# Kernel optimization log

Measured on AMD Instinct MI355X. Metric: run time of the kernel, lower is better.

The kernel has to match this reference:

```python
import jax, jax.numpy as jnp
import numpy as np

B, N, K = 4, 4096, 16
C_IN = 128
EPS = 1e-5


def setup_inputs() -> dict:
    key = jax.random.key(0)
    ks = jax.random.split(key, 8)
    c0 = 2 * C_IN + 3  # concat channels: pos_diff(3) + feat2(128) + feat1(128)
    return {
        "pos1": jax.random.normal(ks[0], (B, 3, N), jnp.float32),
        "pos2": jax.random.normal(ks[1], (B, 3, N), jnp.float32),
        "feature1": jax.random.normal(ks[2], (B, C_IN, N), jnp.float32),
        "feature2": jax.random.normal(ks[3], (B, C_IN, N), jnp.float32),
        "W0": jax.random.normal(ks[4], (128, c0), jnp.float32) * 0.05,
        "W1": jax.random.normal(ks[5], (128, 128), jnp.float32) * 0.05,
        "W2": jax.random.normal(ks[6], (128, 128), jnp.float32) * 0.05,
        "g0": jnp.ones((128,), jnp.float32),
        "g1": jnp.ones((128,), jnp.float32),
        "g2": jnp.ones((128,), jnp.float32),
        "b0": jnp.zeros((128,), jnp.float32),
        "b1": jnp.zeros((128,), jnp.float32),
        "b2": jnp.zeros((128,), jnp.float32),
    }


def _knn_idx(pos1, pos2, k):
    # pos1, pos2: (B, 3, N).  For each point in pos1, k nearest points in pos2.
    p1 = pos1.transpose(0, 2, 1)  # (B, N, 3)
    p2 = pos2.transpose(0, 2, 1)  # (B, M, 3)
    d = (jnp.sum(p1 * p1, -1, keepdims=True)
         + jnp.sum(p2 * p2, -1)[:, None, :]
         - 2.0 * jnp.einsum("bnc,bmc->bnm", p1, p2))  # (B, N, M) squared dists
    _, idx = jax.lax.top_k(-d, k)  # (B, N, K)
    return idx


def _group(x, idx):
    # x: (B, C, M), idx: (B, N, K) -> (B, C, N, K)
    xt = x.transpose(0, 2, 1)  # (B, M, C)
    g = jax.vmap(lambda a, i: a[i])(xt, idx)  # (B, N, K, C)
    return g.transpose(0, 3, 1, 2)


def _conv_bn_relu(x, W, g, b):
    # 1x1 conv (no bias) + BatchNorm2d (training: batch stats, biased var) + ReLU
    y = jnp.einsum("oc,bcnk->bonk", W, x)
    mu = jnp.mean(y, axis=(0, 2, 3), keepdims=True)
    var = jnp.var(y, axis=(0, 2, 3), keepdims=True)
    yn = (y - mu) * jax.lax.rsqrt(var + EPS)
    return jax.nn.relu(yn * g[None, :, None, None] + b[None, :, None, None])


def reference(pos1, pos2, feature1, feature2, W0, W1, W2, g0, g1, g2, b0, b1, b2):
    idx = _knn_idx(pos1, pos2, K)                      # (B, N, K)
    pos2_g = _group(pos2, idx)                         # (B, 3, N, K)
    pos_diff = pos2_g - pos1[:, :, :, None]
    feat2_g = _group(feature2, idx)                    # (B, C, N, K)
    feat1_rep = jnp.broadcast_to(feature1[:, :, :, None], (B, C_IN, N, K))
    x = jnp.concatenate([pos_diff, feat2_g, feat1_rep], axis=1)  # (B, 2C+3, N, K)
    x = _conv_bn_relu(x, W0, g0, b0)
    x = _conv_bn_relu(x, W1, g1, b1)
    x = _conv_bn_relu(x, W2, g2, b2)
    feat1_new = jnp.max(x, axis=-1)                    # (B, mlp[-1], N)
    return (pos1, feat1_new)
```

## Files before the change

### kernel.cpp

```cpp
#include <hip/hip_runtime.h>

#define B_ 4
#define N_ 4096
#define K_ 16
#define C_ 128
#define NQ (B_*N_)
#define COLS_TOT (NQ*K_)
#define CNT_F 262144.0f
#define EPS_ 1e-5f

typedef __attribute__((ext_vector_type(8))) short short8;
typedef __attribute__((ext_vector_type(4))) float f4;
typedef __attribute__((ext_vector_type(4))) int i4;

__device__ __forceinline__ unsigned short f2bf(float f){
  unsigned u = __builtin_bit_cast(unsigned, f);
  u = u + 0x7fffu + ((u >> 16) & 1u);
  return (unsigned short)(u >> 16);
}
__device__ __forceinline__ float bf2f(unsigned short h){
  return __builtin_bit_cast(float, ((unsigned)h) << 16);
}
__device__ __forceinline__ int swzc(int c){ return c ^ ((c >> 3) & 7); }

__global__ __launch_bounds__(256) void wconv(
    const float* __restrict__ W0, const float* __restrict__ W1, const float* __restrict__ W2,
    unsigned short* __restrict__ W0b, unsigned short* __restrict__ W0c,
    unsigned short* __restrict__ W1b, unsigned short* __restrict__ W2b)
{
  int i = blockIdx.x * 256 + threadIdx.x;
  int sel = i >> 14, r = i & 16383;
  int o = r >> 7, c = r & 127;
  float v; unsigned short* dst;
  if (sel == 0)      { v = W0[o*259 + 3   + c]; dst = W0b; }
  else if (sel == 1) { v = W0[o*259 + 131 + c]; dst = W0c; }
  else if (sel == 2) { v = W1[o*128 + c];       dst = W1b; }
  else               { v = W2[o*128 + c];       dst = W2b; }
  dst[r] = f2bf(v);
}

__global__ __launch_bounds__(256) void knn_chunk(
    const float* __restrict__ pos1, const float* __restrict__ pos2,
    float* __restrict__ kdout, int* __restrict__ kiout)
{
  __shared__ __align__(16) float pts[256*4];
  int bx = blockIdx.x;
  int b = bx >> 8, rest = bx & 255, ngrp = rest >> 4, chunk = rest & 15;
  int t = threadIdx.x;
  int m0 = chunk * 256;
  const float* p2 = pos2 + (size_t)b*3*N_;
  {
    int m = m0 + t;
    float x = p2[m], y = p2[N_ + m], z = p2[2*N_ + m];
    float sq = __fadd_rn(__fadd_rn(__fmul_rn(x,x), __fmul_rn(y,y)), __fmul_rn(z,z));
    f4 v; v.x = x; v.y = y; v.z = z; v.w = sq;
    *(f4*)(pts + t*4) = v;
  }
  __syncthreads();

  int n = ngrp*256 + t;
  const float* p1 = pos1 + (size_t)b*3*N_;
  float qx = p1[n], qy = p1[N_ + n], qz = p1[2*N_ + n];
  float qs = __fadd_rn(__fadd_rn(__fmul_rn(qx,qx), __fmul_rn(qy,qy)), __fmul_rn(qz,qz));

  float kd[16]; int ki[16];
  #pragma unroll
  for (int j = 0; j < 16; ++j){ kd[j] = 3.4e38f; ki[j] = 0; }
  float worst = 3.4e38f;
  float pd = 0.f; int pi = 0; bool pv = false;

  auto flush = [&](){
    float d0 = pv ? pd : 3.4e38f; int i0 = pi;
    #pragma unroll
    for (int j = 15; j >= 1; --j){
      bool cj = kd[j] > d0, cm = kd[j-1] > d0;
      kd[j] = cj ? (cm ? kd[j-1] : d0) : kd[j];
      ki[j] = cj ? (cm ? ki[j-1] : i0) : ki[j];
    }
    { bool c0 = kd[0] > d0; kd[0] = c0 ? d0 : kd[0]; ki[0] = c0 ? i0 : ki[0]; }
    worst = kd[15]; pv = false;
  };

  for (int bt = 0; bt < 32; ++bt){
    #pragma unroll
    for (int e = 0; e < 8; ++e){
      int it = bt*8 + e;
      f4 c = *(const f4*)(pts + it*4);
      float dot = __builtin_fmaf(qz, c.z,
                    __builtin_fmaf(qy, c.y, __fmul_rn(qx, c.x)));
      float d = __fsub_rn(__fadd_rn(qs, c.w), __fmul_rn(2.0f, dot));
      bool pass = d < worst;
      if (__any(pass && pv)) flush();
      if (pass){ pd = d; pi = m0 + it; pv = true; }
    }
    if (__any(pv)) flush();
  }
  if (__any(pv)) flush();

  int q = b*N_ + n;
  #pragma unroll
  for (int j = 0; j < 16; ++j){
    kdout[(size_t)q*256 + chunk*16 + j] = kd[j];
    kiout[(size_t)q*256 + chunk*16 + j] = ki[j];
  }
}

__global__ __launch_bounds__(256) void knn_merge(
    const float* __restrict__ kdin, const int* __restrict__ kiin, int* __restrict__ idxout)
{
  int q = blockIdx.x*256 + threadIdx.x;
  float kd[16]; int ki[16];
  #pragma unroll
  for (int j = 0; j < 16; ++j){ kd[j] = 3.4e38f; ki[j] = 0; }
  const float* dsrc = kdin + (size_t)q*256;
  const int*   isrc = kiin + (size_t)q*256;
  for (int l = 0; l < 16; ++l){
    bool dead = false;
    #pragma unroll 1
    for (int s4 = 0; s4 < 4; ++s4){
      if (__all(dead)) break;
      f4 dv = *(const f4*)(dsrc + l*16 + s4*4);
      i4 iv = *(const i4*)(isrc + l*16 + s4*4);
      #pragma unroll
      for (int e = 0; e < 4; ++e){
        float d0 = dv[e]; int i0 = iv[e];
        bool ins = !dead && (kd[15] > d0);
        dead = dead || !ins;
        if (ins){
          #pragma unroll
          for (int j = 15; j >= 1; --j){
            bool cj = kd[j] > d0, cm = kd[j-1] > d0;
            kd[j] = cj ? (cm ? kd[j-1] : d0) : kd[j];
            ki[j] = cj ? (cm ? ki[j-1] : i0) : ki[j];
          }
          bool c0 = kd[0] > d0; kd[0] = c0 ? d0 : kd[0]; ki[0] = c0 ? i0 : ki[0];
        }
      }
    }
  }
  #pragma unroll
  for (int j = 0; j < 16; ++j) idxout[(size_t)q*16 + j] = ki[j];
}

__global__ __launch_bounds__(256) void p1_gemm(
    const float* __restrict__ feat2, const float* __restrict__ feat1,
    const unsigned short* __restrict__ W0b, const unsigned short* __restrict__ W0c,
    float* __restrict__ F2t, float* __restrict__ PREt)
{
  __shared__ __align__(16) unsigned short X[16*128*8];
  int bid = blockIdx.x;
  int sel = bid >> 7;
  const float* src = sel ? feat1 : feat2;
  const unsigned short* W = sel ? W0c : W0b;
  float* dst = sel ? PREt : F2t;
  int c0 = (bid & 127) * 128;
  int b = c0 >> 12, mm0 = c0 & 4095;
  int t = threadIdx.x;
  {
    int ch = t >> 1, half = t & 1;
    const float* s = src + ((size_t)b*C_ + ch)*N_ + mm0 + half*64;
    int kb = ch >> 3, e = ch & 7;
    for (int mi = 0; mi < 64; ++mi){
      int col = half*64 + mi;
      X[kb*1024 + swzc(col)*8 + e] = f2bf(s[mi]);
    }
  }
  int lane = t & 63, w = t >> 6;
  int or0 = (w >> 1)*64, c0w = (w & 1)*64;
  int lr = lane & 15, lg = lane >> 4;
  short8 af[4][4];
  #pragma unroll
  for (int ks = 0; ks < 4; ++ks)
    #pragma unroll
    for (int i = 0; i < 4; ++i)
      af[ks][i] = *(const short8*)(W + (or0 + 16*i + lr)*128 + ks*32 + 8*lg);
  __syncthreads();

  f4 acc[4][4] = {};
  #pragma unroll
  for (int ks = 0; ks < 4; ++ks){
    short8 bfr[4];
    #pragma unroll
    for (int j = 0; j < 4; ++j)
      bfr[j] = *(const short8*)(X + (ks*4 + lg)*1024 + swzc(c0w + 16*j + lr)*8);
    #pragma unroll
    for (int i = 0; i < 4; ++i)
      #pragma unroll
      for (int j = 0; j < 4; ++j)
        acc[i][j] = __builtin_amdgcn_mfma_f32_16x16x32_bf16(af[ks][i], bfr[j], acc[i][j], 0, 0, 0);
  }
  #pragma unroll
  for (int i = 0; i < 4; ++i)
    #pragma unroll
    for (int j = 0; j < 4; ++j){
      int col = c0 + c0w + 16*j + lr;
      *(f4*)(dst + (size_t)col*C_ + or0 + 16*i + 4*lg) = acc[i][j];
    }
}

__global__ __launch_bounds__(256) void k3_y0(
    const float* __restrict__ pos1, const float* __restrict__ pos2,
    const float* __restrict__ W0, const int* __restrict__ idx,
    const float* __restrict__ F2t, const float* __restrict__ PREt,
    unsigned short* __restrict__ ybuf, float* __restrict__ partials)
{
  __shared__ float w0a[384];
  __shared__ float ldsS[256];
  int t = threadIdx.x;
  for (int i = t; i < 384; i += 256) w0a[i] = W0[(i/3)*259 + (i%3)];
  __syncthreads();
  int cloc = t & 15, chg = t >> 4, ch0 = chg*8;
  float wx[8], wy[8], wz[8];
  #pragma unroll
  for (int e = 0; e < 8; ++e){
    wx[e] = w0a[(ch0+e)*3]; wy[e] = w0a[(ch0+e)*3+1]; wz[e] = w0a[(ch0+e)*3+2];
  }
  float s1[8] = {}, s2[8] = {};
  int base = blockIdx.x * 256;
  for (int it = 0; it < 16; ++it){
    int col = base + it*16 + cloc;
    int nabs = col >> 4;
    int b = nabs >> 12, n = nabs & 4095;
    int m = idx[col];
    float dx = pos2[(size_t)(b*3+0)*N_ + m] - pos1[(size_t)(b*3+0)*N_ + n];
    float dy = pos2[(size_t)(b*3+1)*N_ + m] - pos1[(size_t)(b*3+1)*N_ + n];
    float dz = pos2[(size_t)(b*3+2)*N_ + m] - pos1[(size_t)(b*3+2)*N_ + n];
    const float* f2 = F2t  + ((size_t)b*N_ + m)*C_ + ch0;
    const float* pr = PREt + ((size_t)b*N_ + n)*C_ + ch0;
    short8 sv;
    #pragma unroll
    for (int e = 0; e < 8; ++e){
      float y = f2[e] + pr[e];
      y = fmaf(wx[e], dx, y); y = fmaf(wy[e], dy, y); y = fmaf(wz[e], dz, y);
      s1[e] += y; s2[e] = fmaf(y, y, s2[e]);
      sv[e] = (short)f2bf(y);
    }
    *(short8*)(ybuf + (size_t)col*C_ + ch0) = sv;
  }
  #pragma unroll
  for (int e = 0; e < 8; ++e){
    float a = s1[e], q = s2[e];
    #pragma unroll
    for (int sft = 1; sft < 16; sft <<= 1){ a += __shfl_xor(a, sft); q += __shfl_xor(q, sft); }
    if (cloc == 0){ ldsS[ch0 + e] = a; ldsS[128 + ch0 + e] = q; }
  }
  __syncthreads();
  partials[(size_t)blockIdx.x*256 + t] = ldsS[t];
}

__global__ __launch_bounds__(256) void reduce1(const float* __restrict__ partials,
                                               float* __restrict__ partial2)
{
  int t = threadIdx.x, r0 = blockIdx.x*32;
  float a = 0.f;
  #pragma unroll 4
  for (int i = 0; i < 32; ++i) a += partials[(size_t)(r0+i)*256 + t];
  partial2[(size_t)blockIdx.x*256 + t] = a;
}

__global__ __launch_bounds__(256) void finalize(const float* __restrict__ partial2, int rows,
    const float* __restrict__ g, const float* __restrict__ bb,
    float* __restrict__ cA, float* __restrict__ cB)
{
  __shared__ float sh[256];
  int t = threadIdx.x;
  float a = 0.f;
  for (int i = 0; i < rows; ++i) a += partial2[(size_t)i*256 + t];
  sh[t] = a;
  __syncthreads();
  if (t < 128){
    float mu = sh[t] / CNT_F;
    float var = sh[128 + t] / CNT_F - mu*mu;
    float A = g[t] * rsqrtf(var + EPS_);
    cA[t] = A; cB[t] = bb[t] - mu*A;
  }
}

template<int LAST>
__global__ __launch_bounds__(256,2) void layer_gemm(
    unsigned short* ybuf,
    const unsigned short* __restrict__ Wbf,
    const float* __restrict__ cA, const float* __restrict__ cB,
    float* __restrict__ y2max,
    float* __restrict__ partials)
{
  __shared__ __align__(16) char lds[38912];
  unsigned short* X = (unsigned short*)lds;
  float* ldsA = (float*)(lds + 34816);
  float* ldsB = ldsA + 128;
  float* ldsS = ldsB + 128;
  int t = threadIdx.x;
  int c0 = blockIdx.x * 128;
  if (t < 128){ ldsA[t] = cA[t]; ldsB[t] = cB[t]; }
  ldsS[t] = 0.f; ldsS[256 + t] = 0.f;

  int lane = t & 63, w = t >> 6;
  int or0 = (w >> 1)*64, c0w = (w & 1)*64;
  int lr = lane & 15, lg = lane >> 4;
  short8 af[4][4];
  #pragma unroll
  for (int ks = 0; ks < 4; ++ks)
    #pragma unroll
    for (int i = 0; i < 4; ++i)
      af[ks][i] = *(const short8*)(Wbf + (or0 + 16*i + lr)*128 + ks*32 + 8*lg);
  __syncthreads();

  {
    int colL = t >> 1, half = t & 1;
    const unsigned short* src = ybuf + (size_t)(c0 + colL)*128 + half*64;
    int sc = swzc(colL);
    #pragma unroll
    for (int cc = 0; cc < 8; ++cc){
      int ch0 = half*64 + cc*8;
      short8 yv = *(const short8*)(src + cc*8);
      short8 xv;
      #pragma unroll
      for (int e = 0; e < 8; ++e){
        float f = bf2f((unsigned short)yv[e]);
        float v = fmaf(f, ldsA[ch0 + e], ldsB[ch0 + e]);
        v = v > 0.f ? v : 0.f;
        xv[e] = (short)f2bf(v);
      }
      *(short8*)(X + (ch0 >> 3)*1024 + sc*8) = xv;
    }
  }
  __syncthreads();

  f4 acc[4][4] = {};
  #pragma unroll
  for (int ks = 0; ks < 4; ++ks){
    short8 bfr[4];
    #pragma unroll
    for (int j = 0; j < 4; ++j)
      bfr[j] = *(const short8*)(X + (ks*4 + lg)*1024 + swzc(c0w + 16*j + lr)*8);
    #pragma unroll
    for (int i = 0; i < 4; ++i)
      #pragma unroll
      for (int j = 0; j < 4; ++j)
        acc[i][j] = __builtin_amdgcn_mfma_f32_16x16x32_bf16(af[ks][i], bfr[j], acc[i][j], 0, 0, 0);
  }

  #pragma unroll
  for (int i = 0; i < 4; ++i)
    #pragma unroll
    for (int e = 0; e < 4; ++e){
      float a0 = acc[i][0][e], a1 = acc[i][1][e], a2 = acc[i][2][e], a3 = acc[i][3][e];
      float s1 = (a0 + a1) + (a2 + a3);
      float s2 = (a0*a0 + a1*a1) + (a2*a2 + a3*a3);
      #pragma unroll
      for (int sft = 1; sft < 16; sft <<= 1){ s1 += __shfl_xor(s1, sft); s2 += __shfl_xor(s2, sft); }
      if (lr == 0){
        int o = or0 + 16*i + 4*lg + e;
        ldsS[(w & 1)*256 + o] = s1;
        ldsS[(w & 1)*256 + 128 + o] = s2;
      }
    }

  if (!LAST){
    __syncthreads();
    unsigned short* OT = (unsigned short*)lds;
    #pragma unroll
    for (int i = 0; i < 4; ++i)
      #pragma unroll
      for (int j = 0; j < 4; ++j){
        int col = c0w + 16*j + lr;
        int o0 = or0 + 16*i + 4*lg;
        unsigned long long pv =
            (unsigned long long)f2bf(acc[i][j][0])
          | ((unsigned long long)f2bf(acc[i][j][1]) << 16)
          | ((unsigned long long)f2bf(acc[i][j][2]) << 32)
          | ((unsigned long long)f2bf(acc[i][j][3]) << 48);
        *(unsigned long long*)(OT + col*136 + o0) = pv;
      }
    __syncthreads();
    {
      int colL = t >> 1, half = t & 1;
      unsigned short* dst = ybuf + (size_t)(c0 + colL)*128 + half*64;
      #pragma unroll
      for (int cc = 0; cc < 8; ++cc){
        short8 v = *(const short8*)(OT + colL*136 + half*64 + cc*8);
        *(short8*)(dst + cc*8) = v;
      }
    }
    __syncthreads();
    partials[(size_t)blockIdx.x*256 + t] = ldsS[t] + ldsS[256 + t];
  } else {
    float keep[4][4] = {};
    #pragma unroll
    for (int j = 0; j < 4; ++j)
      #pragma unroll
      for (int i = 0; i < 4; ++i)
        #pragma unroll
        for (int e = 0; e < 4; ++e){
          float v = acc[i][j][e];
          #pragma unroll
          for (int sft = 1; sft < 16; sft <<= 1) v = fmaxf(v, __shfl_xor(v, sft));
          if (lr == j) keep[i][e] = v;
        }
    if (lr < 4){
      int colg = c0 + c0w + 16*lr;
      int nabs = colg >> 4;
      float* dst = y2max + (size_t)nabs*C_;
      #pragma unroll
      for (int i = 0; i < 4; ++i){
        f4 v; v.x = keep[i][0]; v.y = keep[i][1]; v.z = keep[i][2]; v.w = keep[i][3];
        *(f4*)(dst + or0 + 16*i + 4*lg) = v;
      }
    }
    __syncthreads();
    partials[(size_t)blockIdx.x*256 + t] = ldsS[t] + ldsS[256 + t];
  }
}

__global__ __launch_bounds__(256) void k7_out(
    const float* __restrict__ y2max, const float* __restrict__ cA,
    const float* __restrict__ cB, float* __restrict__ outF)
{
  __shared__ __align__(16) float T[128*65];
  int t = threadIdx.x, bid = blockIdx.x;
  int b = bid >> 6, n0 = (bid & 63)*64;
  {
    int nl = t >> 2, o0 = (t & 3)*32;
    const float* src = y2max + ((size_t)b*N_ + n0 + nl)*C_ + o0;
    #pragma unroll
    for (int jj = 0; jj < 8; ++jj){
      f4 v = *(const f4*)(src + jj*4);
      T[(o0 + jj*4 + 0)*65 + nl] = v.x;
      T[(o0 + jj*4 + 1)*65 + nl] = v.y;
      T[(o0 + jj*4 + 2)*65 + nl] = v.z;
      T[(o0 + jj*4 + 3)*65 + nl] = v.w;
    }
  }
  __syncthreads();
  {
    int o = t >> 1, half = t & 1;
    float A = cA[o], Bb = cB[o];
    float* dst = outF + ((size_t)b*C_ + o)*N_ + n0 + half*32;
    #pragma unroll
    for (int jj = 0; jj < 8; ++jj){
      f4 v;
      float x0 = fmaf(T[o*65 + half*32 + jj*4+0], A, Bb);
      float x1 = fmaf(T[o*65 + half*32 + jj*4+1], A, Bb);
      float x2 = fmaf(T[o*65 + half*32 + jj*4+2], A, Bb);
      float x3 = fmaf(T[o*65 + half*32 + jj*4+3], A, Bb);
      v.x = x0 > 0.f ? x0 : 0.f; v.y = x1 > 0.f ? x1 : 0.f;
      v.z = x2 > 0.f ? x2 : 0.f; v.w = x3 > 0.f ? x3 : 0.f;
      *(f4*)(dst + jj*4) = v;
    }
  }
}

extern "C" void kernel_launch(void* const* d_in, const int* in_sizes, int n_in,
                              void* d_out, int out_size, void* d_ws, size_t ws_size,
                              hipStream_t stream)
{
  (void)in_sizes; (void)n_in; (void)out_size; (void)ws_size;
  const float* pos1  = (const float*)d_in[0];
  const float* pos2  = (const float*)d_in[1];
  const float* feat1 = (const float*)d_in[2];
  const float* feat2 = (const float*)d_in[3];
  const float* W0 = (const float*)d_in[4];
  const float* W1 = (const float*)d_in[5];
  const float* W2 = (const float*)d_in[6];
  const float* g0 = (const float*)d_in[7];
  const float* g1 = (const float*)d_in[8];
  const float* g2 = (const float*)d_in[9];
  const float* b0 = (const float*)d_in[10];
  const float* b1 = (const float*)d_in[11];
  const float* b2 = (const float*)d_in[12];

  char* ws = (char*)d_ws;
  size_t off = 0;
  auto alloc = [&](size_t bytes){ size_t r = off; off += (bytes + 255) & ~(size_t)255; return r; };
  int*   idx     = (int*)  (ws + alloc((size_t)COLS_TOT*4));
  float* F2t     = (float*)(ws + alloc((size_t)NQ*C_*4));
  float* PREt    = (float*)(ws + alloc((size_t)NQ*C_*4));
  unsigned short* ybuf = (unsigned short*)(ws + alloc((size_t)COLS_TOT*C_*2));
  float* y2max   = (float*)(ws + alloc((size_t)NQ*C_*4));
  float* partials= (float*)(ws + alloc((size_t)2048*256*4));
  float* partial2= (float*)(ws + alloc((size_t)64*256*4));
  float* coef    = (float*)(ws + alloc((size_t)6*128*4));
  unsigned short* W0bb = (unsigned short*)(ws + alloc(16384*2));
  unsigned short* W0cb = (unsigned short*)(ws + alloc(16384*2));
  unsigned short* W1b  = (unsigned short*)(ws + alloc(16384*2));
  unsigned short* W2b  = (unsigned short*)(ws + alloc(16384*2));

  float* knn_d = (float*)ybuf;
  int*   knn_i = (int*)((char*)ybuf + (size_t)NQ*256*4);

  float* cA0 = coef,       *cB0 = coef + 128;
  float* cA1 = coef + 256, *cB1 = coef + 384;
  float* cA2 = coef + 512, *cB2 = coef + 640;

  wconv<<<256, 256, 0, stream>>>(W0, W1, W2, W0bb, W0cb, W1b, W2b);
  knn_chunk<<<1024, 256, 0, stream>>>(pos1, pos2, knn_d, knn_i);
  knn_merge<<<64, 256, 0, stream>>>(knn_d, knn_i, idx);
  p1_gemm<<<256, 256, 0, stream>>>(feat2, feat1, W0bb, W0cb, F2t, PREt);
  k3_y0<<<1024, 256, 0, stream>>>(pos1, pos2, W0, idx, F2t, PREt, ybuf, partials);
  reduce1<<<32, 256, 0, stream>>>(partials, partial2);
  finalize<<<1, 256, 0, stream>>>(partial2, 32, g0, b0, cA0, cB0);
  layer_gemm<0><<<2048, 256, 0, stream>>>(ybuf, W1b, cA0, cB0, nullptr, partials);
  reduce1<<<64, 256, 0, stream>>>(partials, partial2);
  finalize<<<1, 256, 0, stream>>>(partial2, 64, g1, b1, cA1, cB1);
  layer_gemm<1><<<2048, 256, 0, stream>>>(ybuf, W2b, cA1, cB1, y2max, partials);
  reduce1<<<64, 256, 0, stream>>>(partials, partial2);
  finalize<<<1, 256, 0, stream>>>(partial2, 64, g2, b2, cA2, cB2);
  k7_out<<<256, 256, 0, stream>>>(y2max, cA2, cB2, (float*)d_out + (size_t)B_*3*N_);
  hipMemcpyAsync(d_out, d_in[0], (size_t)B_*3*N_*4, hipMemcpyDeviceToDevice, stream);
}
```

Before: 410.4 us.

## Morton-sort KNN queries, simplify top-k insert, fuse layer-0 recompute into layer-1 GEMM

Adds a per-batch bitonic sort of query points by Morton code so each KNN wavefront holds spatially nearby queries. The goal is less divergence and more early rejection in the candidate loop. The KNN insertion is rewritten to insert immediately behind a wave-wide any() check instead of using a deferred pending-candidate flush. Layer 0 no longer writes its bf16 activations: a stats-only pass computes the batch-norm statistics, and the layer-1 GEMM recomputes layer 0 on the fly from the gathered features, removing one full write and read of ybuf. The costs are an extra sort kernel, the layer-0 arithmetic done twice, and more work inside the GEMM kernel.

```diff
diff --git a/kernel.cpp b/kernel.cpp
--- a/kernel.cpp
+++ b/kernel.cpp
@@ -22,6 +22,15 @@
   return __builtin_bit_cast(float, ((unsigned)h) << 16);
 }
 __device__ __forceinline__ int swzc(int c){ return c ^ ((c >> 3) & 7); }
+
+__device__ __forceinline__ unsigned spread3(unsigned v){
+  v &= 0xFFu;
+  v = (v | (v << 16)) & 0x030000FFu;
+  v = (v | (v <<  8)) & 0x0300F00Fu;
+  v = (v | (v <<  4)) & 0x030C30C3u;
+  v = (v | (v <<  2)) & 0x09249249u;
+  return v;
+}
 
 __global__ __launch_bounds__(256) void wconv(
     const float* __restrict__ W0, const float* __restrict__ W1, const float* __restrict__ W2,
@@ -39,8 +48,43 @@
   dst[r] = f2bf(v);
 }
 
+__global__ __launch_bounds__(1024) void sortq(
+    const float* __restrict__ pos1, int* __restrict__ perm)
+{
+  __shared__ unsigned long long key[4096];
+  int b = blockIdx.x, t = threadIdx.x;
+  const float* p1 = pos1 + (size_t)b*3*N_;
+  for (int i = t; i < 4096; i += 1024){
+    float x = p1[i], y = p1[N_+i], z = p1[2*N_+i];
+    unsigned qx = (unsigned)(int)fminf(fmaxf((x+4.f)*32.f, 0.f), 255.f);
+    unsigned qy = (unsigned)(int)fminf(fmaxf((y+4.f)*32.f, 0.f), 255.f);
+    unsigned qz = (unsigned)(int)fminf(fmaxf((z+4.f)*32.f, 0.f), 255.f);
+    unsigned m = spread3(qx) | (spread3(qy) << 1) | (spread3(qz) << 2);
+    key[i] = ((unsigned long long)m << 32) | (unsigned)i;
+  }
+  __syncthreads();
+  for (int k = 2; k <= 4096; k <<= 1){
+    for (int j = k >> 1; j > 0; j >>= 1){
+      #pragma unroll 1
+      for (int s = 0; s < 2; ++s){
+        int pid = s*1024 + t;
+        int i = (pid & (j-1)) | ((pid & ~(j-1)) << 1);
+        int p = i | j;
+        bool up = ((i & k) == 0);
+        unsigned long long a = key[i], c = key[p];
+        bool sw = up ? (a > c) : (a < c);
+        if (sw){ key[i] = c; key[p] = a; }
+      }
+      __syncthreads();
+    }
+  }
+  for (int i = t; i < 4096; i += 1024)
+    perm[b*4096 + i] = (int)(unsigned)(key[i] & 0xFFFFFFFFu);
+}
+
 __global__ __launch_bounds__(256) void knn_chunk(
     const float* __restrict__ pos1, const float* __restrict__ pos2,
+    const int* __restrict__ perm,
     float* __restrict__ kdout, int* __restrict__ kiout)
 {
   __shared__ __align__(16) float pts[256*4];
@@ -58,7 +102,7 @@
   }
   __syncthreads();
 
-  int n = ngrp*256 + t;
+  int n = perm[b*4096 + ngrp*256 + t];
   const float* p1 = pos1 + (size_t)b*3*N_;
   float qx = p1[n], qy = p1[N_ + n], qz = p1[2*N_ + n];
   float qs = __fadd_rn(__fadd_rn(__fmul_rn(qx,qx), __fmul_rn(qy,qy)), __fmul_rn(qz,qz));
@@ -66,36 +110,30 @@
   float kd[16]; int ki[16];
   #pragma unroll
   for (int j = 0; j < 16; ++j){ kd[j] = 3.4e38f; ki[j] = 0; }
-  float worst = 3.4e38f;
-  float pd = 0.f; int pi = 0; bool pv = false;
-
-  auto flush = [&](){
-    float d0 = pv ? pd : 3.4e38f; int i0 = pi;
-    #pragma unroll
-    for (int j = 15; j >= 1; --j){
-      bool cj = kd[j] > d0, cm = kd[j-1] > d0;
-      kd[j] = cj ? (cm ? kd[j-1] : d0) : kd[j];
-      ki[j] = cj ? (cm ? ki[j-1] : i0) : ki[j];
-    }
-    { bool c0 = kd[0] > d0; kd[0] = c0 ? d0 : kd[0]; ki[0] = c0 ? i0 : ki[0]; }
-    worst = kd[15]; pv = false;
-  };
-
-  for (int bt = 0; bt < 32; ++bt){
-    #pragma unroll
-    for (int e = 0; e < 8; ++e){
-      int it = bt*8 + e;
-      f4 c = *(const f4*)(pts + it*4);
-      float dot = __builtin_fmaf(qz, c.z,
-                    __builtin_fmaf(qy, c.y, __fmul_rn(qx, c.x)));
-      float d = __fsub_rn(__fadd_rn(qs, c.w), __fmul_rn(2.0f, dot));
-      bool pass = d < worst;
-      if (__any(pass && pv)) flush();
-      if (pass){ pd = d; pi = m0 + it; pv = true; }
-    }
-    if (__any(pv)) flush();
-  }
-  if (__any(pv)) flush();
+
+  #pragma unroll 4
+  for (int it = 0; it < 256; ++it){
+    f4 c = *(const f4*)(pts + it*4);
+    float dot = __builtin_fmaf(qz, c.z,
+                  __builtin_fmaf(qy, c.y, __fmul_rn(qx, c.x)));
+    float d = __builtin_fmaf(-2.0f, dot, __fadd_rn(qs, c.w));
+    bool pass = d < kd[15];
+    if (__any(pass)){
+      if (pass){
+        int i0 = m0 + it;
+        bool cm = kd[14] > d;
+        kd[15] = cm ? kd[14] : d;  ki[15] = cm ? ki[14] : i0;
+        #pragma unroll
+        for (int j = 14; j >= 1; --j){
+          bool cj = cm;
+          cm = kd[j-1] > d;
+          kd[j] = cj ? (cm ? kd[j-1] : d) : kd[j];
+          ki[j] = cj ? (cm ? ki[j-1] : i0) : ki[j];
+        }
+        kd[0] = cm ? d : kd[0];  ki[0] = cm ? i0 : ki[0];
+      }
+    }
+  }
 
   int q = b*N_ + n;
   #pragma unroll
@@ -198,11 +236,11 @@
     }
 }
 
-__global__ __launch_bounds__(256) void k3_y0(
+__global__ __launch_bounds__(256) void k3_stats(
     const float* __restrict__ pos1, const float* __restrict__ pos2,
     const float* __restrict__ W0, const int* __restrict__ idx,
     const float* __restrict__ F2t, const float* __restrict__ PREt,
-    unsigned short* __restrict__ ybuf, float* __restrict__ partials)
+    float* __restrict__ partials)
 {
   __shared__ float w0a[384];
   __shared__ float ldsS[256];
@@ -227,15 +265,12 @@
     float dz = pos2[(size_t)(b*3+2)*N_ + m] - pos1[(size_t)(b*3+2)*N_ + n];
     const float* f2 = F2t  + ((size_t)b*N_ + m)*C_ + ch0;
     const float* pr = PREt + ((size_t)b*N_ + n)*C_ + ch0;
-    short8 sv;
     #pragma unroll
     for (int e = 0; e < 8; ++e){
       float y = f2[e] + pr[e];
       y = fmaf(wx[e], dx, y); y = fmaf(wy[e], dy, y); y = fmaf(wz[e], dz, y);
       s1[e] += y; s2[e] = fmaf(y, y, s2[e]);
-      sv[e] = (short)f2bf(y);
-    }
-    *(short8*)(ybuf + (size_t)col*C_ + ch0) = sv;
+    }
   }
   #pragma unroll
   for (int e = 0; e < 8; ++e){
@@ -276,8 +311,133 @@
   }
 }
 
-template<int LAST>
-__global__ __launch_bounds__(256,2) void layer_gemm(
+__global__ __launch_bounds__(256,2) void layer1_fused(
+    const float* __restrict__ pos1, const float* __restrict__ pos2,
+    const float* __restrict__ W0, const int* __restrict__ idx,
+    const float* __restrict__ F2t, const float* __restrict__ PREt,
+    unsigned short* __restrict__ ybuf,
+    const unsigned short* __restrict__ Wbf,
+    const float* __restrict__ cA, const float* __restrict__ cB,
+    float* __restrict__ partials)
+{
+  __shared__ __align__(16) char lds[40960];
+  unsigned short* X = (unsigned short*)lds;
+  float* ldsA = (float*)(lds + 32768);
+  float* ldsB = ldsA + 128;
+  float* w0a  = ldsB + 128;
+  float* ldsS = w0a + 384;
+  int t = threadIdx.x;
+  int c0 = blockIdx.x * 128;
+  if (t < 128){ ldsA[t] = cA[t]; ldsB[t] = cB[t]; }
+  for (int i = t; i < 384; i += 256) w0a[i] = W0[(i/3)*259 + (i%3)];
+  ldsS[t] = 0.f; ldsS[256 + t] = 0.f;
+  __syncthreads();
+
+  int lane = t & 63, w = t >> 6;
+  int or0 = (w >> 1)*64, c0w = (w & 1)*64;
+  int lr = lane & 15, lg = lane >> 4;
+
+  {
+    int colL = t >> 1, half = t & 1;
+    int col = c0 + colL;
+    int nabs = col >> 4;
+    int b = nabs >> 12, n = nabs & 4095;
+    int m = idx[col];
+    float dx = pos2[(size_t)(b*3+0)*N_ + m] - pos1[(size_t)(b*3+0)*N_ + n];
+    float dy = pos2[(size_t)(b*3+1)*N_ + m] - pos1[(size_t)(b*3+1)*N_ + n];
+    float dz = pos2[(size_t)(b*3+2)*N_ + m] - pos1[(size_t)(b*3+2)*N_ + n];
+    const float* f2 = F2t  + ((size_t)b*N_ + m)*C_ + half*64;
+    const float* pr = PREt + ((size_t)b*N_ + n)*C_ + half*64;
+    int sc = swzc(colL);
+    #pragma unroll
+    for (int cc = 0; cc < 8; ++cc){
+      int ch0 = half*64 + cc*8;
+      f4 a0 = *(const f4*)(f2 + cc*8), a1 = *(const f4*)(f2 + cc*8 + 4);
+      f4 b0 = *(const f4*)(pr + cc*8), b1 = *(const f4*)(pr + cc*8 + 4);
+      short8 xv;
+      #pragma unroll
+      for (int e = 0; e < 8; ++e){
+        int ch = ch0 + e;
+        float fv = (e < 4 ? a0[e] : a1[e-4]);
+        float pv = (e < 4 ? b0[e] : b1[e-4]);
+        float y = fv + pv;
+        y = fmaf(w0a[ch*3], dx, y); y = fmaf(w0a[ch*3+1], dy, y); y = fmaf(w0a[ch*3+2], dz, y);
+        float v = fmaf(y, ldsA[ch], ldsB[ch]);
+        v = v > 0.f ? v : 0.f;
+        xv[e] = (short)f2bf(v);
+      }
+      *(short8*)(X + (ch0 >> 3)*1024 + sc*8) = xv;
+    }
+  }
+
+  short8 af[4][4];
+  #pragma unroll
+  for (int ks = 0; ks < 4; ++ks)
+    #pragma unroll
+    for (int i = 0; i < 4; ++i)
+      af[ks][i] = *(const short8*)(Wbf + (or0 + 16*i + lr)*128 + ks*32 + 8*lg);
+  __syncthreads();
+
+  f4 acc[4][4] = {};
+  #pragma unroll
+  for (int ks = 0; ks < 4; ++ks){
+    short8 bfr[4];
+    #pragma unroll
+    for (int j = 0; j < 4; ++j)
+      bfr[j] = *(const short8*)(X + (ks*4 + lg)*1024 + swzc(c0w + 16*j + lr)*8);
+    #pragma unroll
+    for (int i = 0; i < 4; ++i)
+      #pragma unroll
+      for (int j = 0; j < 4; ++j)
+        acc[i][j] = __builtin_amdgcn_mfma_f32_16x16x32_bf16(af[ks][i], bfr[j], acc[i][j], 0, 0, 0);
+  }
+
+  #pragma unroll
+  for (int i = 0; i < 4; ++i)
+    #pragma unroll
+    for (int e = 0; e < 4; ++e){
+      float a0 = acc[i][0][e], a1 = acc[i][1][e], a2 = acc[i][2][e], a3 = acc[i][3][e];
+      float s1 = (a0 + a1) + (a2 + a3);
+      float s2 = (a0*a0 + a1*a1) + (a2*a2 + a3*a3);
+      #pragma unroll
+      for (int sft = 1; sft < 16; sft <<= 1){ s1 += __shfl_xor(s1, sft); s2 += __shfl_xor(s2, sft); }
+      if (lr == 0){
+        int o = or0 + 16*i + 4*lg + e;
+        ldsS[(w & 1)*256 + o] = s1;
+        ldsS[(w & 1)*256 + 128 + o] = s2;
+      }
+    }
+
+  __syncthreads();
+  unsigned short* OT = (unsigned short*)lds;
+  #pragma unroll
+  for (int i = 0; i < 4; ++i)
+    #pragma unroll
+    for (int j = 0; j < 4; ++j){
+      int col = c0w + 16*j + lr;
+      int o0 = or0 + 16*i + 4*lg;
+      unsigned long long pv =
+          (unsigned long long)f2bf(acc[i][j][0])
+        | ((unsigned long long)f2bf(acc[i][j][1]) << 16)
+        | ((unsigned long long)f2bf(acc[i][j][2]) << 32)
+        | ((unsigned long long)f2bf(acc[i][j][3]) << 48);
+      *(unsigned long long*)(OT + col*136 + o0) = pv;
+    }
+  __syncthreads();
+  {
+    int colL = t >> 1, half = t & 1;
+    unsigned short* dst = ybuf + (size_t)(c0 + colL)*128 + half*64;
+    #pragma unroll
+    for (int cc = 0; cc < 8; ++cc){
+      short8 v = *(const short8*)(OT + colL*136 + half*64 + cc*8);
+      *(short8*)(dst + cc*8) = v;
+    }
+  }
+  __syncthreads();
+  partials[(size_t)blockIdx.x*256 + t] = ldsS[t] + ldsS[256 + t];
+}
+
+__global__ __launch_bounds__(256,2) void layer_gemm_last(
     unsigned short* ybuf,
     const unsigned short* __restrict__ Wbf,
     const float* __restrict__ cA, const float* __restrict__ cB,
@@ -356,60 +516,30 @@
       }
     }
 
-  if (!LAST){
-    __syncthreads();
-    unsigned short* OT = (unsigned short*)lds;
+  float keep[4][4] = {};
+  #pragma unroll
+  for (int j = 0; j < 4; ++j)
     #pragma unroll
     for (int i = 0; i < 4; ++i)
       #pragma unroll
-      for (int j = 0; j < 4; ++j){
-        int col = c0w + 16*j + lr;
-        int o0 = or0 + 16*i + 4*lg;
-        unsigned long long pv =
-            (unsigned long long)f2bf(acc[i][j][0])
-          | ((unsigned long long)f2bf(acc[i][j][1]) << 16)
-          | ((unsigned long long)f2bf(acc[i][j][2]) << 32)
-          | ((unsigned long long)f2bf(acc[i][j][3]) << 48);
-        *(unsigned long long*)(OT + col*136 + o0) = pv;
-      }
-    __syncthreads();
-    {
-      int colL = t >> 1, half = t & 1;
-      unsigned short* dst = ybuf + (size_t)(c0 + colL)*128 + half*64;
-      #pragma unroll
-      for (int cc = 0; cc < 8; ++cc){
-        short8 v = *(const short8*)(OT + colL*136 + half*64 + cc*8);
-        *(short8*)(dst + cc*8) = v;
-      }
-    }
-    __syncthreads();
-    partials[(size_t)blockIdx.x*256 + t] = ldsS[t] + ldsS[256 + t];
-  } else {
-    float keep[4][4] = {};
-    #pragma unroll
-    for (int j = 0; j < 4; ++j)
-      #pragma unroll
-      for (int i = 0; i < 4; ++i)
+      for (int e = 0; e < 4; ++e){
+        float v = acc[i][j][e];
         #pragma unroll
-        for (int e = 0; e < 4; ++e){
-          float v = acc[i][j][e];
-          #pragma unroll
-          for (int sft = 1; sft < 16; sft <<= 1) v = fmaxf(v, __shfl_xor(v, sft));
-          if (lr == j) keep[i][e] = v;
-        }
-    if (lr < 4){
-      int colg = c0 + c0w + 16*lr;
-      int nabs = colg >> 4;
-      float* dst = y2max + (size_t)nabs*C_;
-      #pragma unroll
-      for (int i = 0; i < 4; ++i){
-        f4 v; v.x = keep[i][0]; v.y = keep[i][1]; v.z = keep[i][2]; v.w = keep[i][3];
-        *(f4*)(dst + or0 + 16*i + 4*lg) = v;
-      }
-    }
-    __syncthreads();
-    partials[(size_t)blockIdx.x*256 + t] = ldsS[t] + ldsS[256 + t];
-  }
+        for (int sft = 1; sft < 16; sft <<= 1) v = fmaxf(v, __shfl_xor(v, sft));
+        if (lr == j) keep[i][e] = v;
+      }
+  if (lr < 4){
+    int colg = c0 + c0w + 16*lr;
+    int nabs = colg >> 4;
+    float* dst = y2max + (size_t)nabs*C_;
+    #pragma unroll
+    for (int i = 0; i < 4; ++i){
+      f4 v; v.x = keep[i][0]; v.y = keep[i][1]; v.z = keep[i][2]; v.w = keep[i][3];
+      *(f4*)(dst + or0 + 16*i + 4*lg) = v;
+    }
+  }
+  __syncthreads();
+  partials[(size_t)blockIdx.x*256 + t] = ldsS[t] + ldsS[256 + t];
 }
 
 __global__ __launch_bounds__(256) void k7_out(
@@ -473,6 +603,7 @@
   size_t off = 0;
   auto alloc = [&](size_t bytes){ size_t r = off; off += (bytes + 255) & ~(size_t)255; return r; };
   int*   idx     = (int*)  (ws + alloc((size_t)COLS_TOT*4));
+  int*   perm    = (int*)  (ws + alloc((size_t)NQ*4));
   float* F2t     = (float*)(ws + alloc((size_t)NQ*C_*4));
   float* PREt    = (float*)(ws + alloc((size_t)NQ*C_*4));
   unsigned short* ybuf = (unsigned short*)(ws + alloc((size_t)COLS_TOT*C_*2));
@@ -493,16 +624,18 @@
   float* cA2 = coef + 512, *cB2 = coef + 640;
 
   wconv<<<256, 256, 0, stream>>>(W0, W1, W2, W0bb, W0cb, W1b, W2b);
-  knn_chunk<<<1024, 256, 0, stream>>>(pos1, pos2, knn_d, knn_i);
+  sortq<<<B_, 1024, 0, stream>>>(pos1, perm);
+  knn_chunk<<<1024, 256, 0, stream>>>(pos1, pos2, perm, knn_d, knn_i);
   knn_merge<<<64, 256, 0, stream>>>(knn_d, knn_i, idx);
   p1_gemm<<<256, 256, 0, stream>>>(feat2, feat1, W0bb, W0cb, F2t, PREt);
-  k3_y0<<<1024, 256, 0, stream>>>(pos1, pos2, W0, idx, F2t, PREt, ybuf, partials);
+  k3_stats<<<1024, 256, 0, stream>>>(pos1, pos2, W0, idx, F2t, PREt, partials);
   reduce1<<<32, 256, 0, stream>>>(partials, partial2);
   finalize<<<1, 256, 0, stream>>>(partial2, 32, g0, b0, cA0, cB0);
-  layer_gemm<0><<<2048, 256, 0, stream>>>(ybuf, W1b, cA0, cB0, nullptr, partials);
+  layer1_fused<<<2048, 256, 0, stream>>>(pos1, pos2, W0, idx, F2t, PREt,
+                                          ybuf, W1b, cA0, cB0, partials);
   reduce1<<<64, 256, 0, stream>>>(partials, partial2);
   finalize<<<1, 256, 0, stream>>>(partial2, 64, g1, b1, cA1, cB1);
-  layer_gemm<1><<<2048, 256, 0, stream>>>(ybuf, W2b, cA1, cB1, y2max, partials);
+  layer_gemm_last<<<2048, 256, 0, stream>>>(ybuf, W2b, cA1, cB1, y2max, partials);
   reduce1<<<64, 256, 0, stream>>>(partials, partial2);
   finalize<<<1, 256, 0, stream>>>(partial2, 64, g2, b2, cA2, cB2);
   k7_out<<<256, 256, 0, stream>>>(y2max, cA2, cB2, (float*)d_out + (size_t)B_*3*N_);
```

Result: slower. 519.0 us (+26.5%).
